# Kernel tuning notes

Hardware: AMD Instinct MI355X
Metric: run time of the kernel (lower is better)

The kernel has to match this reference:

```python
import jax, jax.numpy as jnp
import numpy as np

ALPHA = 0.5  # leakage
T, B, I, H = 512, 64, 128, 1024
SCALE = 0.9  # input_scaling
RHO = 0.99   # target spectral radius (approximated by 1/sqrt(H) normal scaling)


def setup_inputs() -> dict:
    key = jax.random.key(0)
    k1, k2, k3, k4, k5 = jax.random.split(key, 5)
    x = jax.random.normal(k1, (T, B, I), dtype=jnp.float32)
    # uniform(-scale, scale) kernel init
    W_in0 = jax.random.uniform(k2, (H, I), jnp.float32, -SCALE, SCALE)
    # normal recurrent init scaled so spectral radius ~= rho (circular law: radius ~ sigma*sqrt(H))
    W_hat0 = jax.random.normal(k3, (H, H), jnp.float32) * (RHO / np.sqrt(H))
    W_in1 = jax.random.uniform(k4, (H, H), jnp.float32, -SCALE, SCALE)
    W_hat1 = jax.random.normal(k5, (H, H), jnp.float32) * (RHO / np.sqrt(H))
    return {"x": x, "W_in0": W_in0, "W_hat0": W_hat0, "W_in1": W_in1, "W_hat1": W_hat1}


def _run_layer(inp, W_in, W_hat):
    # inp: [T, B, F_in]; returns full state trajectory [T, B, H]
    def step(h, x_t):
        pre = x_t @ W_in.T + h @ W_hat.T          # [B, H]
        h_new = (1.0 - ALPHA) * h + ALPHA * jnp.tanh(pre)
        return h_new, h_new

    h0 = jnp.zeros((inp.shape[1], W_hat.shape[0]), dtype=inp.dtype)
    _, ys = jax.lax.scan(step, h0, inp)
    return ys


def reference(x, W_in0, W_hat0, W_in1, W_hat1):
    e0 = _run_layer(x, W_in0, W_hat0)   # layer 0 states [T, B, H]
    e1 = _run_layer(e0, W_in1, W_hat1)  # layer 1 states [T, B, H]
    return jnp.stack([e0, e1], axis=-2)  # [T, B, num_layers, H]
```

## Files before the change

kernel.cpp:

```cpp
#include <hip/hip_runtime.h>
#include <math.h>

#define TSTEPS 512
#define BATCH  64
#define HDIM   1024
#define IDIM   128
#define NBLOCKS 256
#define NTHR   512
#define NCNT   64

typedef __attribute__((ext_vector_type(8))) short bf16x8;
typedef __attribute__((ext_vector_type(4))) float f32x4;
typedef __attribute__((ext_vector_type(4))) unsigned u32x4;

#define WI0HI 0
#define WI0LO (WI0HI + 1024*128)
#define WH0HI (WI0LO + 1024*128)
#define WH0LO (WH0HI + 1024*1024)
#define WI1HI (WH0LO + 1024*1024)
#define WI1LO (WI1HI + 1024*1024)
#define WH1HI (WI1LO + 1024*1024)
#define WH1LO (WH1HI + 1024*1024)
#define WS_USHORTS (WH1LO + 1024*1024)
#define CNT_OFF_BYTES ((size_t)WS_USHORTS * 2)

__device__ __forceinline__ unsigned short bf_hi(float f) {
    unsigned u = __builtin_bit_cast(unsigned, f);
    unsigned r = u + 0x7fffu + ((u >> 16) & 1u);
    return (unsigned short)(r >> 16);
}
__device__ __forceinline__ float bf_tof(unsigned short h) {
    unsigned u = ((unsigned)h) << 16;
    return __builtin_bit_cast(float, u);
}

__device__ __forceinline__ void split8(const float* __restrict__ p,
                                       bf16x8& ah, bf16x8& al) {
    f32x4 a = *(const f32x4*)p, b = *(const f32x4*)(p + 4);
    float fv[8] = {a[0], a[1], a[2], a[3], b[0], b[1], b[2], b[3]};
    u32x4 H, L;
    #pragma unroll
    for (int q = 0; q < 4; ++q) {
        const float f0 = fv[2 * q], f1 = fv[2 * q + 1];
        unsigned h;
        asm("v_cvt_pk_bf16_f32 %0, %1, %2" : "=v"(h) : "v"(f0), "v"(f1));
        const float h0 = __builtin_bit_cast(float, h << 16);
        const float h1 = __builtin_bit_cast(float, h & 0xffff0000u);
        unsigned lo;
        asm("v_cvt_pk_bf16_f32 %0, %1, %2" : "=v"(lo) : "v"(f0 - h0), "v"(f1 - h1));
        H[q] = h; L[q] = lo;
    }
    ah = __builtin_bit_cast(bf16x8, H);
    al = __builtin_bit_cast(bf16x8, L);
}

__device__ __forceinline__ void ks_r(const float* __restrict__ asrc,
                                     bf16x8 bh, bf16x8 bl, f32x4& acc) {
    bf16x8 ah, al;
    split8(asrc, ah, al);
    acc = __builtin_amdgcn_mfma_f32_16x16x32_bf16(ah, bh, acc, 0, 0, 0);
    acc = __builtin_amdgcn_mfma_f32_16x16x32_bf16(al, bh, acc, 0, 0, 0);
    acc = __builtin_amdgcn_mfma_f32_16x16x32_bf16(ah, bl, acc, 0, 0, 0);
}

__global__ void prep_kernel(const float* __restrict__ Wi0, const float* __restrict__ Wh0,
                            const float* __restrict__ Wi1, const float* __restrict__ Wh1,
                            unsigned short* __restrict__ wsU)
{
    const int n = 1024*128 + 3*1024*1024;
    for (int e = blockIdx.x * blockDim.x + threadIdx.x; e < n;
         e += gridDim.x * blockDim.x) {
        const float* src; int idx, hiOff, loOff;
        if (e < 1024*128)            { src = Wi0; idx = e;              hiOff = WI0HI; loOff = WI0LO; }
        else if (e < 1024*128 + 1024*1024)   { src = Wh0; idx = e - 1024*128;   hiOff = WH0HI; loOff = WH0LO; }
        else if (e < 1024*128 + 2*1024*1024) { src = Wi1; idx = e - 1024*128 - 1024*1024; hiOff = WI1HI; loOff = WI1LO; }
        else                         { src = Wh1; idx = e - 1024*128 - 2*1024*1024; hiOff = WH1HI; loOff = WH1LO; }
        float f = src[idx];
        unsigned short h = bf_hi(f);
        wsU[hiOff + idx] = h;
        wsU[loOff + idx] = bf_hi(f - bf_tof(h));
    }
}

__device__ __forceinline__ void grid_barrier(unsigned* cntBase, unsigned epoch) {
    __syncthreads();
    const int tid = (int)threadIdx.x;
    if (tid == 0)
        __hip_atomic_fetch_add(cntBase + (blockIdx.x & (NCNT - 1)) * 16, 1u,
                               __ATOMIC_RELAXED, __HIP_MEMORY_SCOPE_AGENT);
    if (blockIdx.x == 0) {
        if (tid < 64) {
            const unsigned tgt = (NBLOCKS / NCNT) * epoch;
            for (;;) {
                unsigned v = __hip_atomic_load(cntBase + tid * 16, __ATOMIC_RELAXED,
                                               __HIP_MEMORY_SCOPE_AGENT);
                if (__ballot(v >= tgt) == ~0ull) break;
                __builtin_amdgcn_s_sleep(1);
            }
            if (tid == 0)
                __hip_atomic_store(cntBase + NCNT * 16, epoch,
                                   __ATOMIC_RELAXED, __HIP_MEMORY_SCOPE_AGENT);
        }
    } else if (tid == 0) {
        while (__hip_atomic_load(cntBase + NCNT * 16, __ATOMIC_RELAXED,
                                 __HIP_MEMORY_SCOPE_AGENT) < epoch)
            __builtin_amdgcn_s_sleep(1);
    }
    __syncthreads();
}

__global__ __launch_bounds__(NTHR, 2) void reservoir_kernel(
    const float* __restrict__ x, float* __restrict__ out,
    const unsigned short* __restrict__ wsU, unsigned* __restrict__ cnt)
{
    __shared__ f32x4 red[8 * 64];

    const int bid = blockIdx.x;
    const int layer = bid >> 7;
    const int rr  = bid & 127;
    const int jt  = rr >> 1, mh = rr & 1;
    const int tid = (int)threadIdx.x;
    const int w   = __builtin_amdgcn_readfirstlane(tid >> 6);
    const int m2  = w & 1, kh = w >> 1;
    const int l   = tid & 63, lr = l & 15, tq = l >> 4;
    const int jbase = jt * 16;
    const int arow  = mh * 32 + m2 * 16 + lr;

    bf16x8 wfh[16], wfl[16];
    if (layer == 0) {
        const size_t rx = (size_t)(jbase + lr) * IDIM + kh * 32 + tq * 8;
        wfh[0] = *(const bf16x8*)(wsU + WI0HI + rx);
        wfl[0] = *(const bf16x8*)(wsU + WI0LO + rx);
        const size_t rh = (size_t)(jbase + lr) * HDIM + kh * 256 + tq * 8;
        #pragma unroll
        for (int ks = 0; ks < 8; ++ks) {
            wfh[1 + ks] = *(const bf16x8*)(wsU + WH0HI + rh + ks * 32);
            wfl[1 + ks] = *(const bf16x8*)(wsU + WH0LO + rh + ks * 32);
        }
    } else {
        const int hiOff = (kh < 2) ? WI1HI : WH1HI;
        const int loOff = (kh < 2) ? WI1LO : WH1LO;
        const size_t ro = (size_t)(jbase + lr) * HDIM + (kh & 1) * 512 + tq * 8;
        #pragma unroll
        for (int ks = 0; ks < 16; ++ks) {
            wfh[ks] = *(const bf16x8*)(wsU + hiOff + ro + ks * 32);
            wfl[ks] = *(const bf16x8*)(wsU + loOff + ro + ks * 32);
        }
    }

    float hold[4] = {0.f, 0.f, 0.f, 0.f};

    for (int i = 0; i <= TSTEPS; ++i) {
        const int t = layer ? (i - 1) : i;
        const bool valid = layer ? (t >= 0) : (t < TSTEPS);
        if (valid) {
            f32x4 accA = {0.f, 0.f, 0.f, 0.f};
            f32x4 accB = {0.f, 0.f, 0.f, 0.f};
            if (layer == 0) {
                ks_r(x + (size_t)t * (BATCH * IDIM) + arow * IDIM + kh * 32 + tq * 8,
                     wfh[0], wfl[0], accA);
                if (t >= 1) {
                    const float* h0 = out + (size_t)(t - 1) * 131072 + arow * 2048
                                      + kh * 256 + tq * 8;
                    #pragma unroll
                    for (int ks = 0; ks < 8; ++ks)
                        ks_r(h0 + ks * 32, wfh[1 + ks], wfl[1 + ks],
                             (ks & 1) ? accA : accB);
                }
            } else {
                const bool doit = (kh < 2) || (t >= 1);
                if (doit) {
                    const int ts  = (kh < 2) ? t : (t - 1);
                    const float* src = out + (size_t)ts * 131072 + arow * 2048
                                       + ((kh < 2) ? 0 : 1024) + (kh & 1) * 512 + tq * 8;
                    #pragma unroll
                    for (int ks = 0; ks < 16; ++ks)
                        ks_r(src + ks * 32, wfh[ks], wfl[ks],
                             (ks & 1) ? accA : accB);
                }
            }

            red[w * 64 + l] = accA + accB;
            __syncthreads();
            if (w < 2) {
                f32x4 s  = red[(w + 0) * 64 + l];
                f32x4 s1 = red[(w + 2) * 64 + l];
                f32x4 s2 = red[(w + 4) * 64 + l];
                f32x4 s3 = red[(w + 6) * 64 + l];
                #pragma unroll
                for (int r = 0; r < 4; ++r) {
                    const float pre = ((s[r] + s1[r]) + (s2[r] + s3[r]));
                    const float hnew = 0.5f * hold[r] + 0.5f * tanhf(pre);
                    hold[r] = hnew;
                    const int row = mh * 32 + w * 16 + tq * 4 + r;
                    const int col = jbase + lr;
                    float* dst = out + (size_t)t * 131072 + row * 2048 + layer * 1024 + col;
                    __hip_atomic_store(dst, hnew, __ATOMIC_RELAXED, __HIP_MEMORY_SCOPE_AGENT);
                }
            }
            __syncthreads();
        }
        if (i < TSTEPS)
            grid_barrier(cnt, (unsigned)(i + 1));
    }
}

extern "C" void kernel_launch(void* const* d_in, const int* in_sizes, int n_in,
                              void* d_out, int out_size, void* d_ws, size_t ws_size,
                              hipStream_t stream) {
    const float* x   = (const float*)d_in[0];
    const float* Wi0 = (const float*)d_in[1];
    const float* Wh0 = (const float*)d_in[2];
    const float* Wi1 = (const float*)d_in[3];
    const float* Wh1 = (const float*)d_in[4];
    float* out = (float*)d_out;
    unsigned short* wsU = (unsigned short*)d_ws;
    unsigned* cnt = (unsigned*)((char*)d_ws + CNT_OFF_BYTES);

    hipMemsetAsync((char*)d_ws + CNT_OFF_BYTES, 0, NCNT * 64 + 64, stream);
    prep_kernel<<<256, 256, 0, stream>>>(Wi0, Wh0, Wi1, Wh1, wsU);

    void* args[] = {(void*)&x, (void*)&out, (void*)&wsU, (void*)&cnt};
    hipLaunchCooperativeKernel((const void*)reservoir_kernel,
                               dim3(NBLOCKS), dim3(NTHR), args, 0, stream);
}
```

Measured before the change: 4.846 ms.

## Split grid barrier into arrive/wait and overlap next-step input projection

Replaces the atomic fetch_add counter barrier with per-block epoch flags: each block stores its epoch, block 0 polls all 256 flags and then writes a separate release flag per block. The barrier is split into arrive and wait phases, and layer 0 computes the next timestep's input projection (x @ W_in) between them, hiding that work behind the barrier latency. This is meant to cut atomic contention and take the x-projection off the critical path between steps. It costs more flag memory and more polling loads in block 0.

New measurement: 4.718 ms. 1.03x faster.

```diff
diff --git a/kernel.cpp b/kernel.cpp
--- a/kernel.cpp
+++ b/kernel.cpp
@@ -7,7 +7,6 @@
 #define IDIM   128
 #define NBLOCKS 256
 #define NTHR   512
-#define NCNT   64
 
 typedef __attribute__((ext_vector_type(8))) short bf16x8;
 typedef __attribute__((ext_vector_type(4))) float f32x4;
@@ -23,6 +22,8 @@
 #define WH1LO (WH1HI + 1024*1024)
 #define WS_USHORTS (WH1LO + 1024*1024)
 #define CNT_OFF_BYTES ((size_t)WS_USHORTS * 2)
+#define FLG_DW (256 * 16)
+#define BAR_BYTES (2 * 256 * 64)
 
 __device__ __forceinline__ unsigned short bf_hi(float f) {
     unsigned u = __builtin_bit_cast(unsigned, f);
@@ -82,27 +83,34 @@
     }
 }
 
-__device__ __forceinline__ void grid_barrier(unsigned* cntBase, unsigned epoch) {
+__device__ __forceinline__ void barrier_arrive(unsigned* cnt, unsigned epoch) {
     __syncthreads();
+    if (threadIdx.x == 0)
+        __hip_atomic_store(cnt + (unsigned)blockIdx.x * 16, epoch,
+                           __ATOMIC_RELAXED, __HIP_MEMORY_SCOPE_AGENT);
+}
+__device__ __forceinline__ void barrier_wait(unsigned* cnt, unsigned epoch) {
     const int tid = (int)threadIdx.x;
-    if (tid == 0)
-        __hip_atomic_fetch_add(cntBase + (blockIdx.x & (NCNT - 1)) * 16, 1u,
-                               __ATOMIC_RELAXED, __HIP_MEMORY_SCOPE_AGENT);
     if (blockIdx.x == 0) {
         if (tid < 64) {
-            const unsigned tgt = (NBLOCKS / NCNT) * epoch;
+            unsigned* flg = cnt + FLG_DW;
             for (;;) {
-                unsigned v = __hip_atomic_load(cntBase + tid * 16, __ATOMIC_RELAXED,
-                                               __HIP_MEMORY_SCOPE_AGENT);
-                if (__ballot(v >= tgt) == ~0ull) break;
+                unsigned v0 = __hip_atomic_load(cnt + (tid      ) * 16, __ATOMIC_RELAXED, __HIP_MEMORY_SCOPE_AGENT);
+                unsigned v1 = __hip_atomic_load(cnt + (tid +  64) * 16, __ATOMIC_RELAXED, __HIP_MEMORY_SCOPE_AGENT);
+                unsigned v2 = __hip_atomic_load(cnt + (tid + 128) * 16, __ATOMIC_RELAXED, __HIP_MEMORY_SCOPE_AGENT);
+                unsigned v3 = __hip_atomic_load(cnt + (tid + 192) * 16, __ATOMIC_RELAXED, __HIP_MEMORY_SCOPE_AGENT);
+                bool ok = (v0 >= epoch) & (v1 >= epoch) & (v2 >= epoch) & (v3 >= epoch);
+                if (__ballot(ok) == ~0ull) break;
                 __builtin_amdgcn_s_sleep(1);
             }
-            if (tid == 0)
-                __hip_atomic_store(cntBase + NCNT * 16, epoch,
+            #pragma unroll
+            for (int q = 0; q < 4; ++q)
+                __hip_atomic_store(flg + (q * 64 + tid) * 16, epoch,
                                    __ATOMIC_RELAXED, __HIP_MEMORY_SCOPE_AGENT);
         }
     } else if (tid == 0) {
-        while (__hip_atomic_load(cntBase + NCNT * 16, __ATOMIC_RELAXED,
+        unsigned* myflag = cnt + FLG_DW + (unsigned)blockIdx.x * 16;
+        while (__hip_atomic_load(myflag, __ATOMIC_RELAXED,
                                  __HIP_MEMORY_SCOPE_AGENT) < epoch)
             __builtin_amdgcn_s_sleep(1);
     }
@@ -149,6 +157,7 @@
     }
 
     float hold[4] = {0.f, 0.f, 0.f, 0.f};
+    f32x4 accX = {0.f, 0.f, 0.f, 0.f};
 
     for (int i = 0; i <= TSTEPS; ++i) {
         const int t = layer ? (i - 1) : i;
@@ -157,8 +166,12 @@
             f32x4 accA = {0.f, 0.f, 0.f, 0.f};
             f32x4 accB = {0.f, 0.f, 0.f, 0.f};
             if (layer == 0) {
-                ks_r(x + (size_t)t * (BATCH * IDIM) + arow * IDIM + kh * 32 + tq * 8,
-                     wfh[0], wfl[0], accA);
+                if (i == 0) {
+                    ks_r(x + (size_t)t * (BATCH * IDIM) + arow * IDIM + kh * 32 + tq * 8,
+                         wfh[0], wfl[0], accA);
+                } else {
+                    accA = accX;
+                }
                 if (t >= 1) {
                     const float* h0 = out + (size_t)(t - 1) * 131072 + arow * 2048
                                       + kh * 256 + tq * 8;
@@ -200,8 +213,16 @@
             }
             __syncthreads();
         }
-        if (i < TSTEPS)
-            grid_barrier(cnt, (unsigned)(i + 1));
+        if (i < TSTEPS) {
+            barrier_arrive(cnt, (unsigned)(i + 1));
+            if (layer == 0 && (i + 1) < TSTEPS) {
+                f32x4 z = {0.f, 0.f, 0.f, 0.f};
+                ks_r(x + (size_t)(i + 1) * (BATCH * IDIM) + arow * IDIM + kh * 32 + tq * 8,
+                     wfh[0], wfl[0], z);
+                accX = z;
+            }
+            barrier_wait(cnt, (unsigned)(i + 1));
+        }
     }
 }
 
@@ -217,7 +238,7 @@
     unsigned short* wsU = (unsigned short*)d_ws;
     unsigned* cnt = (unsigned*)((char*)d_ws + CNT_OFF_BYTES);
 
-    hipMemsetAsync((char*)d_ws + CNT_OFF_BYTES, 0, NCNT * 64 + 64, stream);
+    hipMemsetAsync((char*)d_ws + CNT_OFF_BYTES, 0, BAR_BYTES, stream);
     prep_kernel<<<256, 256, 0, stream>>>(Wi0, Wh0, Wi1, Wh1, wsU);
 
     void* args[] = {(void*)&x, (void*)&out, (void*)&wsU, (void*)&cnt};
```
